# Kernel optimization log

Hardware: AMD Instinct MI355X
Metric: run time of the kernel (lower is better)

The kernel has to match this reference:

```python
import jax, jax.numpy as jnp
import numpy as np

CUTOFF = 5.0
N_RBF = 20
N_NODES, N_EDGES, F = 50000, 200000, 128


def setup_inputs() -> dict:
    key = jax.random.key(0)
    ks = jax.random.split(key, 11)
    inp = {
        "s": jax.random.normal(ks[0], (N_NODES, F), jnp.float32),
        "v": jax.random.normal(ks[1], (N_NODES, 3, F), jnp.float32),
        "rel_pos": jax.random.normal(ks[2], (N_EDGES, 3), jnp.float32),
        "W1": jax.random.normal(ks[3], (F, F), jnp.float32) * 0.05,
        "b1": jnp.zeros((F,), jnp.float32),
        "W2": jax.random.normal(ks[4], (F, 3 * F), jnp.float32) * 0.05,
        "b2": jnp.zeros((3 * F,), jnp.float32),
        "Wr": jax.random.normal(ks[5], (N_RBF, 3 * F), jnp.float32) * 0.05,
        "br": jnp.zeros((3 * F,), jnp.float32),
        "src": jax.random.randint(ks[6], (N_EDGES,), 0, N_NODES),
        "dst": jax.random.randint(ks[7], (N_EDGES,), 0, N_NODES),
    }
    return inp


def reference(s, v, rel_pos, W1, b1, W2, b2, Wr, br, src, dst):
    n_nodes, f = s.shape
    # phi MLP on node scalar features (computed per node, then gathered per edge)
    phi = jax.nn.silu(s @ W1 + b1) @ W2 + b2          # [N, 3F]
    phi_e = phi[src]                                   # [E, 3F]

    d = jnp.linalg.norm(rel_pos, axis=-1)              # [E]
    # sinc-style radial basis: sin(n*pi*d/cutoff)/d, n = 1..N_RBF
    n = jnp.arange(1, N_RBF + 1, dtype=d.dtype)
    rbf = jnp.sin(n * (jnp.pi / CUTOFF) * d[:, None]) / d[:, None]  # [E, 20]
    w_proj = rbf @ Wr + br                             # [E, 3F]
    # cosine cutoff gate
    fcut = 0.5 * (jnp.cos(jnp.pi * d / CUTOFF) + 1.0) * (d < CUTOFF)
    w = w_proj * fcut[:, None]                         # [E, 3F]

    split = w * phi_e                                  # hadamard gate, [E, 3F]
    s_v, s_s, s_r = split[:, :f], split[:, f:2 * f], split[:, 2 * f:]

    dirv = rel_pos / d[:, None]                        # r / ||r||, [E, 3]
    # vector message: gated neighbor vectors + gated directions
    dv = v[src] * s_v[:, None, :] + dirv[:, :, None] * s_r[:, None, :]  # [E,3,F]

    out_s = jax.ops.segment_sum(s_s, dst, num_segments=n_nodes)  # [N, F]
    out_v = jax.ops.segment_sum(dv, dst, num_segments=n_nodes)   # [N, 3, F]
    return out_v, out_s
```

## Files before the change

kernel.cpp:

```cpp
#include <hip/hip_runtime.h>
#include <math.h>

#define N_NODES_C 50000
#define N_EDGES_C 200000
#define FDIM 128
#define NRBF 20
#define CUT 5.0f
#define SC_BLK 196
#define GBLOCKS 6250
#define BATCH 32

typedef short  bf16x8 __attribute__((ext_vector_type(8)));
typedef float  f32x4  __attribute__((ext_vector_type(4)));
typedef unsigned int u32x3 __attribute__((ext_vector_type(3)));
typedef _Float16 f16x2 __attribute__((ext_vector_type(2)));

__device__ __forceinline__ unsigned short f32_to_bf16(float f) {
    unsigned u = __float_as_uint(f);
    unsigned r = (u + 0x7FFFu + ((u >> 16) & 1u)) >> 16;
    return (unsigned short)r;
}
__device__ __forceinline__ float bf16_to_f32(unsigned short h) {
    return __uint_as_float(((unsigned)h) << 16);
}
__device__ __forceinline__ unsigned short f16_bits(float x) {
    _Float16 h = (_Float16)x;
    unsigned short b;
    __builtin_memcpy(&b, &h, 2);
    return b;
}
__device__ __forceinline__ f16x2 u2h2(unsigned u) {
    f16x2 r;
    __builtin_memcpy(&r, &u, 4);
    return r;
}
__device__ __forceinline__ bf16x8 pack_bf16x8(f32x4 a, f32x4 b) {
    bf16x8 r;
    r[0] = (short)f32_to_bf16(a[0]); r[1] = (short)f32_to_bf16(a[1]);
    r[2] = (short)f32_to_bf16(a[2]); r[3] = (short)f32_to_bf16(a[3]);
    r[4] = (short)f32_to_bf16(b[0]); r[5] = (short)f32_to_bf16(b[1]);
    r[6] = (short)f32_to_bf16(b[2]); r[7] = (short)f32_to_bf16(b[3]);
    return r;
}

__global__ __launch_bounds__(256) void prep_all_kernel(
    const float* __restrict__ W1, const float* __restrict__ W2,
    const float* __restrict__ Wr, unsigned short* __restrict__ W1t,
    unsigned short* __restrict__ W2t, unsigned* __restrict__ wrh)
{
    int i = blockIdx.x * 256 + threadIdx.x;
    if (i < 128 * 128) {
        int n = i >> 7, k = i & 127;
        W1t[i] = f32_to_bf16(W1[k * 128 + n]);
    } else if (i < 128 * 128 + 384 * 128) {
        int j = i - 128 * 128;
        int n = j >> 7, k = j & 127;
        W2t[j] = f32_to_bf16(W2[k * 384 + n]);
    } else {
        int idx = i - (128 * 128 + 384 * 128);
        if (idx < 128 * 30) {
            int f  = idx / 30;
            int r  = idx % 30;
            int sec = r / 10, kp = r % 10;
            int col = sec * 128 + f;
            unsigned lo = f16_bits(Wr[(2 * kp)     * 384 + col]);
            unsigned hi = f16_bits(Wr[(2 * kp + 1) * 384 + col]);
            wrh[idx] = lo | (hi << 16);
        }
    }
}

__global__ __launch_bounds__(256) void vpack_kernel(
    const float* __restrict__ v, unsigned short* __restrict__ pv)
{
    const int total = N_NODES_C * 128;
    for (int idx = blockIdx.x * 256 + threadIdx.x; idx < total;
         idx += gridDim.x * 256) {
        int n = idx >> 7, f = idx & 127;
        const float* vr = v + (size_t)n * 384;
        unsigned short v0 = f32_to_bf16(__builtin_nontemporal_load(vr + f));
        unsigned short v1 = f32_to_bf16(__builtin_nontemporal_load(vr + 128 + f));
        unsigned short v2 = f32_to_bf16(__builtin_nontemporal_load(vr + 256 + f));
        char* base = (char*)pv + (size_t)n * 1536 + (size_t)f * 12;
        *(unsigned short*)(base + 6) = v0;
        *(unsigned*)(base + 8) = (unsigned)v1 | ((unsigned)v2 << 16);
    }
}

__global__ __launch_bounds__(256) void mlp1w_kernel(
    const float* __restrict__ s, const unsigned short* __restrict__ W1t,
    const float* __restrict__ b1, unsigned short* __restrict__ h)
{
    __shared__ unsigned short w1lds[128 * 136];

    const int tid = threadIdx.x;
#pragma unroll
    for (int j = 0; j < 8; ++j) {
        int fi = tid + j * 256;
        int row  = fi >> 4;
        int colq = fi & 15;
        *(float4*)&w1lds[row * 136 + colq * 8] =
            *(const float4*)(W1t + (size_t)fi * 8);
    }
    __syncthreads();

    const int wv = tid >> 6, lane = tid & 63;
    const int m0 = blockIdx.x * 64 + wv * 16;
    const int lr = lane & 15, lg = lane >> 4;
    int arow = m0 + lr; if (arow >= N_NODES_C) arow = N_NODES_C - 1;

    f32x4 acc[8];
#pragma unroll
    for (int nt = 0; nt < 8; ++nt) acc[nt] = (f32x4){0.f, 0.f, 0.f, 0.f};

#pragma unroll
    for (int kt = 0; kt < 4; ++kt) {
        const int k0 = kt * 32 + lg * 8;
        const f32x4* ap = (const f32x4*)(s + (size_t)arow * 128 + k0);
        f32x4 a0 = __builtin_nontemporal_load(ap);
        f32x4 a1 = __builtin_nontemporal_load(ap + 1);
        bf16x8 af = pack_bf16x8(a0, a1);
#pragma unroll
        for (int nt = 0; nt < 8; ++nt) {
            bf16x8 bf = *(const bf16x8*)&w1lds[(nt * 16 + lr) * 136 + k0];
            acc[nt] = __builtin_amdgcn_mfma_f32_16x16x32_bf16(af, bf, acc[nt], 0, 0, 0);
        }
    }

    const int crow = m0 + lg * 4;
#pragma unroll
    for (int nt = 0; nt < 8; ++nt) {
        int col = nt * 16 + lr;
        float bb = b1[col];
#pragma unroll
        for (int r = 0; r < 4; ++r) {
            int m = crow + r;
            if (m < N_NODES_C) {
                float x = acc[nt][r] + bb;
                x = x / (1.f + __expf(-x));
                h[(size_t)m * 128 + col] = f32_to_bf16(x);
            }
        }
    }
}

__global__ __launch_bounds__(256) void mlp2p_kernel(
    const unsigned short* __restrict__ h, const unsigned short* __restrict__ W2t,
    const float* __restrict__ b2, unsigned short* __restrict__ pv)
{
    __shared__ unsigned short wlds[2][3 * 16 * 136];

    const int tid = threadIdx.x;
    const int wv = tid >> 6, lane = tid & 63;
    const int rg = wv & 1;
    const int hf = wv >> 1;
    const int m0 = blockIdx.x * 32 + rg * 16;
    const int lr = lane & 15, lg = lane >> 4;
    int arow = m0 + lr; if (arow >= N_NODES_C) arow = N_NODES_C - 1;

    bf16x8 af2[4];
#pragma unroll
    for (int kt = 0; kt < 4; ++kt)
        af2[kt] = *(const bf16x8*)(h + (size_t)arow * 128 + kt * 32 + lg * 8);

    const int crow = m0 + lg * 4;

    for (int t = 0; t < 4; ++t) {
        __syncthreads();
#pragma unroll
        for (int j = 0; j < 6; ++j) {
            int fi = tid + j * 256;
            int half = (fi >= 768) ? 1 : 0;
            int rem  = fi - half * 768;
            int c    = rem >> 8;
            int r2   = rem & 255;
            int row  = r2 >> 4;
            int colq = r2 & 15;
            int nt   = half * 4 + t;
            *(float4*)&wlds[half][(c * 16 + row) * 136 + colq * 8] =
                *(const float4*)(W2t +
                    ((size_t)(c * 128 + nt * 16 + row) * 128 + colq * 8));
        }
        __syncthreads();

        const unsigned short* W = wlds[hf];
        f32x4 a0 = (f32x4){0.f, 0.f, 0.f, 0.f};
        f32x4 a1 = (f32x4){0.f, 0.f, 0.f, 0.f};
        f32x4 a2 = (f32x4){0.f, 0.f, 0.f, 0.f};
#pragma unroll
        for (int kt = 0; kt < 4; ++kt) {
            const int k0 = kt * 32 + lg * 8;
            bf16x8 bf0 = *(const bf16x8*)&W[(      lr) * 136 + k0];
            bf16x8 bf1 = *(const bf16x8*)&W[(16 +  lr) * 136 + k0];
            bf16x8 bf2 = *(const bf16x8*)&W[(32 +  lr) * 136 + k0];
            a0 = __builtin_amdgcn_mfma_f32_16x16x32_bf16(af2[kt], bf0, a0, 0, 0, 0);
            a1 = __builtin_amdgcn_mfma_f32_16x16x32_bf16(af2[kt], bf1, a1, 0, 0, 0);
            a2 = __builtin_amdgcn_mfma_f32_16x16x32_bf16(af2[kt], bf2, a2, 0, 0, 0);
        }

        const int col = (hf * 4 + t) * 16 + lr;
        const float bb0 = b2[col], bb1 = b2[128 + col], bb2 = b2[256 + col];
#pragma unroll
        for (int r = 0; r < 4; ++r) {
            int m = crow + r;
            if (m < N_NODES_C) {
                unsigned p0 = f32_to_bf16(a0[r] + bb0);
                unsigned p1 = f32_to_bf16(a1[r] + bb1);
                unsigned short p2 = f32_to_bf16(a2[r] + bb2);
                char* base = (char*)pv + (size_t)m * 1536 + (size_t)col * 12;
                *(unsigned*)(base) = p0 | (p1 << 16);
                *(unsigned short*)(base + 4) = p2;
            }
        }
    }
}

__global__ __launch_bounds__(256) void count_kernel(
    const int* __restrict__ dst, int* __restrict__ counts)
{
    int e = blockIdx.x * 256 + threadIdx.x;
    if (e < N_EDGES_C) atomicAdd(counts + dst[e], 1);
}

__global__ __launch_bounds__(256) void scan1_kernel(
    const int* __restrict__ counts, int* __restrict__ row_tmp,
    int* __restrict__ partial)
{
    __shared__ int sm[256];
    const int t = threadIdx.x;
    const int idx = blockIdx.x * 256 + t;
    int c = (idx < N_NODES_C) ? counts[idx] : 0;
    int x = c;
    sm[t] = x;
    __syncthreads();
#pragma unroll
    for (int off = 1; off < 256; off <<= 1) {
        int y = (t >= off) ? sm[t - off] : 0;
        __syncthreads();
        x += y;
        sm[t] = x;
        __syncthreads();
    }
    if (idx < N_NODES_C) row_tmp[idx] = x - c;
    if (t == 255) partial[blockIdx.x] = x;
}

__global__ __launch_bounds__(256) void scan2_kernel(
    const int* __restrict__ partial, int* __restrict__ poffs)
{
    __shared__ int sm[256];
    const int t = threadIdx.x;
    int c = (t < SC_BLK) ? partial[t] : 0;
    int x = c;
    sm[t] = x;
    __syncthreads();
#pragma unroll
    for (int off = 1; off < 256; off <<= 1) {
        int y = (t >= off) ? sm[t - off] : 0;
        __syncthreads();
        x += y;
        sm[t] = x;
        __syncthreads();
    }
    if (t < SC_BLK) poffs[t] = x - c;
}

__global__ __launch_bounds__(256) void scan3_kernel(
    const int* __restrict__ row_tmp, const int* __restrict__ poffs,
    int* __restrict__ row_ptr, int* __restrict__ row_fill)
{
    const int idx = blockIdx.x * 256 + threadIdx.x;
    if (idx < N_NODES_C) {
        int rp = row_tmp[idx] + poffs[blockIdx.x];
        row_ptr[idx]  = rp;
        row_fill[idx] = rp;
    }
    if (idx == 0) row_ptr[N_NODES_C] = N_EDGES_C;
}

__global__ __launch_bounds__(256) void fill_kernel(
    const float* __restrict__ rel_pos, const int* __restrict__ src,
    const int* __restrict__ dst, int* __restrict__ row_fill,
    float* __restrict__ e_meta)
{
    int e = blockIdx.x * 256 + threadIdx.x;
    if (e >= N_EDGES_C) return;

    int pos = atomicAdd(row_fill + dst[e], 1);

    float x = rel_pos[3 * e + 0];
    float y = rel_pos[3 * e + 1];
    float z = rel_pos[3 * e + 2];
    float d = sqrtf(x * x + y * y + z * z);
    float invd = 1.0f / d;

    float s1 = 0.f, c1 = 0.f, fcut = 0.f, amp = 0.f;
    if (d < CUT) {
        sincosf((3.14159265358979f / CUT) * d, &s1, &c1);
        fcut = 0.5f * (c1 + 1.0f);
        amp  = invd * fcut;
    }

    float rb[NRBF];
    float sk = s1, ck = c1;
#pragma unroll
    for (int k = 0; k < NRBF; ++k) {
        rb[k] = sk * amp;
        float sn = sk * c1 + ck * s1;
        ck = ck * c1 - sk * s1;
        sk = sn;
    }

    unsigned pk[10];
#pragma unroll
    for (int kp = 0; kp < 10; ++kp)
        pk[kp] = (unsigned)f16_bits(rb[2 * kp]) | ((unsigned)f16_bits(rb[2 * kp + 1]) << 16);

    float4* mp = (float4*)(e_meta + (size_t)pos * 16);
    mp[0] = make_float4(x * invd, y * invd, z * invd, fcut);
    mp[1] = make_float4(__uint_as_float(pk[0]), __uint_as_float(pk[1]),
                        __uint_as_float(pk[2]), __uint_as_float(pk[3]));
    mp[2] = make_float4(__uint_as_float(pk[4]), __uint_as_float(pk[5]),
                        __uint_as_float(pk[6]), __uint_as_float(pk[7]));
    mp[3] = make_float4(__uint_as_float(pk[8]), __uint_as_float(pk[9]),
                        __int_as_float(src[e]), 0.f);
}

#define COMPUTE_E(M_, U)                                                       \
    {                                                                          \
        const float4 m0 = *(const float4*)(M_);                                \
        const unsigned* mu_ = (const unsigned*)((M_) + 4);                     \
        float w0 = m0.w * br0, w1 = m0.w * br1, w2 = m0.w * br2;               \
        _Pragma("unroll")                                                      \
        for (int kp = 0; kp < 10; ++kp) {                                      \
            f16x2 rh = u2h2(mu_[kp]);                                          \
            w0 = __builtin_amdgcn_fdot2(rh, u2h2(wrp0[kp]), w0, false);        \
            w1 = __builtin_amdgcn_fdot2(rh, u2h2(wrp1[kp]), w1, false);        \
            w2 = __builtin_amdgcn_fdot2(rh, u2h2(wrp2[kp]), w2, false);        \
        }                                                                      \
        float P0 = bf16_to_f32((unsigned short)((U).x & 0xFFFFu));             \
        float P1 = bf16_to_f32((unsigned short)((U).x >> 16));                 \
        float P2 = bf16_to_f32((unsigned short)((U).y & 0xFFFFu));             \
        float V0 = bf16_to_f32((unsigned short)((U).y >> 16));                 \
        float V1 = bf16_to_f32((unsigned short)((U).z & 0xFFFFu));             \
        float V2 = bf16_to_f32((unsigned short)((U).z >> 16));                 \
        float sv = w0 * P0;                                                    \
        float ss = w1 * P1;                                                    \
        float sr = w2 * P2;                                                    \
        acc_s  += ss;                                                          \
        acc_v0 += V0 * sv + m0.x * sr;                                         \
        acc_v1 += V1 * sv + m0.y * sr;                                         \
        acc_v2 += V2 * sv + m0.z * sr;                                         \
    }

#define LOADPV(U, SI)                                                          \
    U = *(const u32x3*)((const char*)pv + (size_t)(SI) * 1536 + (size_t)f * 12);

#define STORE_NODE(N_, AS, A0, A1, A2)                                         \
    {                                                                          \
        __builtin_nontemporal_store(AS, &out_s[(size_t)(N_) * 128 + f]);       \
        __builtin_nontemporal_store(A0, &out_v[(size_t)(N_) * 384 +       f]); \
        __builtin_nontemporal_store(A1, &out_v[(size_t)(N_) * 384 + 128 + f]); \
        __builtin_nontemporal_store(A2, &out_v[(size_t)(N_) * 384 + 256 + f]); \
    }

#define BOUNDARY(GE)                                                           \
    if ((GE) + 1 == end_cur) {                                                 \
        STORE_NODE(cur, acc_s, acc_v0, acc_v1, acc_v2);                        \
        acc_s = acc_v0 = acc_v1 = acc_v2 = 0.f;                                \
        ++cur;                                                                 \
        while (cur < nhi) {                                                    \
            int ne_ = row_ptr[cur + 1];                                        \
            if (ne_ != (GE) + 1) { end_cur = ne_; break; }                     \
            STORE_NODE(cur, 0.f, 0.f, 0.f, 0.f);                               \
            ++cur;                                                             \
        }                                                                      \
    }

__global__ __launch_bounds__(128) void gather_packed_kernel(
    const unsigned short* __restrict__ pv, const unsigned* __restrict__ wrh,
    const float* __restrict__ br, const int* __restrict__ row_ptr,
    const float* __restrict__ e_meta,
    float* __restrict__ out_v, float* __restrict__ out_s)
{
    __shared__ float meta_lds[2][BATCH * 16];

    const int f = threadIdx.x;
    const int gid = blockIdx.x;
    const int chunk = (N_NODES_C + GBLOCKS - 1) / GBLOCKS;
    const int nlo = gid * chunk;
    if (nlo >= N_NODES_C) return;
    const int nhi = min(nlo + chunk, N_NODES_C);

    unsigned wrp0[10], wrp1[10], wrp2[10];
    {
        const unsigned* wp = wrh + (size_t)f * 30;
#pragma unroll
        for (int i = 0; i < 10; ++i) {
            wrp0[i] = wp[i];
            wrp1[i] = wp[10 + i];
            wrp2[i] = wp[20 + i];
        }
#pragma unroll
        for (int i = 0; i < 10; ++i)
            asm volatile("" : "+v"(wrp0[i]), "+v"(wrp1[i]), "+v"(wrp2[i]));
    }
    const float br0 = br[f], br1 = br[128 + f], br2 = br[256 + f];

    const int gbeg = row_ptr[nlo];
    const int gend = row_ptr[nhi];
    const int nedge = gend - gbeg;

    float acc_s = 0.f, acc_v0 = 0.f, acc_v1 = 0.f, acc_v2 = 0.f;

    int cur = nlo;
    while (cur < nhi && row_ptr[cur + 1] == gbeg) {
        STORE_NODE(cur, 0.f, 0.f, 0.f, 0.f);
        ++cur;
    }
    int end_cur = (cur < nhi) ? row_ptr[cur + 1] : gbeg;

    if (nedge > 0) {
        const f32x4* src0 = (const f32x4*)(e_meta + (size_t)gbeg * 16);
        f32x4 s0 = __builtin_nontemporal_load(src0 + threadIdx.x);
        ((f32x4*)meta_lds[0])[threadIdx.x] = s0;
    }
    __syncthreads();

    const int total_batches = (nedge + BATCH - 1) / BATCH;
    for (int b = 0; b < total_batches; ++b) {
        const int bstart = b * BATCH;
        const int bcount = min(BATCH, nedge - bstart);
        const bool have_next = (b + 1 < total_batches);

        f32x4 st;
        if (have_next) {
            const f32x4* srcn =
                (const f32x4*)(e_meta + (size_t)(gbeg + bstart + BATCH) * 16);
            st = __builtin_nontemporal_load(srcn + threadIdx.x);
        }

        const float* Mb = meta_lds[b & 1];

        u32x3 uA, uB;
        {
            int si = ((const int*)Mb)[14];
            LOADPV(uA, si);
        }

        int t = 0;
        while (t < bcount) {
            if (t + 1 < bcount) {
                int si = ((const int*)(Mb + (t + 1) * 16))[14];
                LOADPV(uB, si);
            }
            COMPUTE_E(Mb + t * 16, uA);
            BOUNDARY(gbeg + bstart + t);
            ++t; if (t >= bcount) break;

            if (t + 1 < bcount) {
                int si = ((const int*)(Mb + (t + 1) * 16))[14];
                LOADPV(uA, si);
            }
            COMPUTE_E(Mb + t * 16, uB);
            BOUNDARY(gbeg + bstart + t);
            ++t;
        }

        if (have_next) ((f32x4*)meta_lds[(b + 1) & 1])[threadIdx.x] = st;
        __syncthreads();
    }
}

extern "C" void kernel_launch(void* const* d_in, const int* in_sizes, int n_in,
                              void* d_out, int out_size, void* d_ws, size_t ws_size,
                              hipStream_t stream)
{
    const float* s  = (const float*)d_in[0];
    const float* v  = (const float*)d_in[1];
    const float* rp = (const float*)d_in[2];
    const float* W1 = (const float*)d_in[3];
    const float* b1 = (const float*)d_in[4];
    const float* W2 = (const float*)d_in[5];
    const float* b2 = (const float*)d_in[6];
    const float* Wr = (const float*)d_in[7];
    const float* br = (const float*)d_in[8];
    const int* src  = (const int*)d_in[9];
    const int* dst  = (const int*)d_in[10];

    float* out   = (float*)d_out;
    float* out_v = out;
    float* out_s = out + (size_t)N_NODES_C * 3 * FDIM;

    char* ws = (char*)d_ws;
    float* e_meta = (float*)ws;                 ws += ((size_t)N_EDGES_C * 16 + 256) * sizeof(float);
    unsigned short* W1t = (unsigned short*)ws;  ws += (size_t)128 * 128 * sizeof(unsigned short);
    unsigned short* W2t = (unsigned short*)ws;  ws += (size_t)384 * 128 * sizeof(unsigned short);
    unsigned* wrh = (unsigned*)ws;              ws += (size_t)128 * 30 * sizeof(unsigned);
    int* counts   = (int*)ws;                   ws += (size_t)N_NODES_C * sizeof(int);
    int* row_ptr  = (int*)ws;                   ws += (size_t)(N_NODES_C + 4) * sizeof(int);
    int* row_fill = (int*)ws;                   ws += (size_t)N_NODES_C * sizeof(int);
    int* row_tmp  = (int*)ws;                   ws += (size_t)N_NODES_C * sizeof(int);
    int* partial  = (int*)ws;                   ws += (size_t)256 * sizeof(int);
    int* poffs    = (int*)ws;                   ws += (size_t)256 * sizeof(int);
    unsigned short* h = (unsigned short*)ws;    ws += (size_t)N_NODES_C * 128 * sizeof(unsigned short);
    unsigned short* pv = (unsigned short*)ws;

    hipMemsetAsync(counts, 0, (size_t)N_NODES_C * sizeof(int), stream);

    count_kernel<<<(N_EDGES_C + 255) / 256, 256, 0, stream>>>(dst, counts);
    scan1_kernel<<<SC_BLK, 256, 0, stream>>>(counts, row_tmp, partial);
    scan2_kernel<<<1, 256, 0, stream>>>(partial, poffs);
    scan3_kernel<<<SC_BLK, 256, 0, stream>>>(row_tmp, poffs, row_ptr, row_fill);
    fill_kernel<<<(N_EDGES_C + 255) / 256, 256, 0, stream>>>(rp, src, dst, row_fill, e_meta);

    prep_all_kernel<<<272, 256, 0, stream>>>(W1, W2, Wr, W1t, W2t, wrh);
    vpack_kernel<<<4096, 256, 0, stream>>>(v, pv);
    mlp1w_kernel<<<(N_NODES_C + 63) / 64, 256, 0, stream>>>(s, W1t, b1, h);
    mlp2p_kernel<<<(N_NODES_C + 31) / 32, 256, 0, stream>>>(h, W2t, b2, pv);

    gather_packed_kernel<<<GBLOCKS, 128, 0, stream>>>(pv, wrh, br, row_ptr,
                                                      e_meta, out_v, out_s);
}
```

Before: 200.7 us.

## Merge independent preprocessing kernels into two block-partitioned launches

Folds vpack, count, and weight prep into one launch whose blocks are split by role. It also folds mlp1 and the edge fill into a second launch, cutting the launch count from 10 to 7. The goal is to remove launch gaps and let independent work run at the same time on the GPU. The cost is that k5 blocks all reserve the shared memory sized for the MLP branch, which may lower occupancy for the fill blocks.

```diff
diff --git a/kernel.cpp b/kernel.cpp
--- a/kernel.cpp
+++ b/kernel.cpp
@@ -10,6 +10,12 @@
 #define GBLOCKS 6250
 #define BATCH 32
 
+#define K1_VP 4096
+#define K1_CT 782
+#define K1_PR 272
+#define K5_ML 782
+#define K5_FL 782
+
 typedef short  bf16x8 __attribute__((ext_vector_type(8)));
 typedef float  f32x4  __attribute__((ext_vector_type(4)));
 typedef unsigned int u32x3 __attribute__((ext_vector_type(3)));
@@ -43,104 +49,214 @@
     return r;
 }
 
-__global__ __launch_bounds__(256) void prep_all_kernel(
+__global__ __launch_bounds__(256) void k1_kernel(
+    const float* __restrict__ v, unsigned short* __restrict__ pv,
+    const int* __restrict__ dst, int* __restrict__ counts,
     const float* __restrict__ W1, const float* __restrict__ W2,
     const float* __restrict__ Wr, unsigned short* __restrict__ W1t,
     unsigned short* __restrict__ W2t, unsigned* __restrict__ wrh)
 {
-    int i = blockIdx.x * 256 + threadIdx.x;
-    if (i < 128 * 128) {
-        int n = i >> 7, k = i & 127;
-        W1t[i] = f32_to_bf16(W1[k * 128 + n]);
-    } else if (i < 128 * 128 + 384 * 128) {
-        int j = i - 128 * 128;
-        int n = j >> 7, k = j & 127;
-        W2t[j] = f32_to_bf16(W2[k * 384 + n]);
+    const int bid = blockIdx.x;
+    const int tid = threadIdx.x;
+
+    if (bid < K1_VP) {
+        const int total = N_NODES_C * 128;
+        for (int idx = bid * 256 + tid; idx < total; idx += K1_VP * 256) {
+            int n = idx >> 7, f = idx & 127;
+            const float* vr = v + (size_t)n * 384;
+            unsigned short v0 = f32_to_bf16(__builtin_nontemporal_load(vr + f));
+            unsigned short v1 = f32_to_bf16(__builtin_nontemporal_load(vr + 128 + f));
+            unsigned short v2 = f32_to_bf16(__builtin_nontemporal_load(vr + 256 + f));
+            char* base = (char*)pv + (size_t)n * 1536 + (size_t)f * 12;
+            *(unsigned short*)(base + 6) = v0;
+            *(unsigned*)(base + 8) = (unsigned)v1 | ((unsigned)v2 << 16);
+        }
+    } else if (bid < K1_VP + K1_CT) {
+        int e = (bid - K1_VP) * 256 + tid;
+        if (e < N_EDGES_C) atomicAdd(counts + dst[e], 1);
     } else {
-        int idx = i - (128 * 128 + 384 * 128);
-        if (idx < 128 * 30) {
-            int f  = idx / 30;
-            int r  = idx % 30;
-            int sec = r / 10, kp = r % 10;
-            int col = sec * 128 + f;
-            unsigned lo = f16_bits(Wr[(2 * kp)     * 384 + col]);
-            unsigned hi = f16_bits(Wr[(2 * kp + 1) * 384 + col]);
-            wrh[idx] = lo | (hi << 16);
-        }
-    }
-}
-
-__global__ __launch_bounds__(256) void vpack_kernel(
-    const float* __restrict__ v, unsigned short* __restrict__ pv)
-{
-    const int total = N_NODES_C * 128;
-    for (int idx = blockIdx.x * 256 + threadIdx.x; idx < total;
-         idx += gridDim.x * 256) {
-        int n = idx >> 7, f = idx & 127;
-        const float* vr = v + (size_t)n * 384;
-        unsigned short v0 = f32_to_bf16(__builtin_nontemporal_load(vr + f));
-        unsigned short v1 = f32_to_bf16(__builtin_nontemporal_load(vr + 128 + f));
-        unsigned short v2 = f32_to_bf16(__builtin_nontemporal_load(vr + 256 + f));
-        char* base = (char*)pv + (size_t)n * 1536 + (size_t)f * 12;
-        *(unsigned short*)(base + 6) = v0;
-        *(unsigned*)(base + 8) = (unsigned)v1 | ((unsigned)v2 << 16);
-    }
-}
-
-__global__ __launch_bounds__(256) void mlp1w_kernel(
+        int i = (bid - K1_VP - K1_CT) * 256 + tid;
+        if (i < 128 * 128) {
+            int n = i >> 7, k = i & 127;
+            W1t[i] = f32_to_bf16(W1[k * 128 + n]);
+        } else if (i < 128 * 128 + 384 * 128) {
+            int j = i - 128 * 128;
+            int n = j >> 7, k = j & 127;
+            W2t[j] = f32_to_bf16(W2[k * 384 + n]);
+        } else {
+            int idx = i - (128 * 128 + 384 * 128);
+            if (idx < 128 * 30) {
+                int f  = idx / 30;
+                int r  = idx % 30;
+                int sec = r / 10, kp = r % 10;
+                int col = sec * 128 + f;
+                unsigned lo = f16_bits(Wr[(2 * kp)     * 384 + col]);
+                unsigned hi = f16_bits(Wr[(2 * kp + 1) * 384 + col]);
+                wrh[idx] = lo | (hi << 16);
+            }
+        }
+    }
+}
+
+__global__ __launch_bounds__(256) void scan1_kernel(
+    const int* __restrict__ counts, int* __restrict__ row_tmp,
+    int* __restrict__ partial)
+{
+    __shared__ int sm[256];
+    const int t = threadIdx.x;
+    const int idx = blockIdx.x * 256 + t;
+    int c = (idx < N_NODES_C) ? counts[idx] : 0;
+    int x = c;
+    sm[t] = x;
+    __syncthreads();
+#pragma unroll
+    for (int off = 1; off < 256; off <<= 1) {
+        int y = (t >= off) ? sm[t - off] : 0;
+        __syncthreads();
+        x += y;
+        sm[t] = x;
+        __syncthreads();
+    }
+    if (idx < N_NODES_C) row_tmp[idx] = x - c;
+    if (t == 255) partial[blockIdx.x] = x;
+}
+
+__global__ __launch_bounds__(256) void scan2_kernel(
+    const int* __restrict__ partial, int* __restrict__ poffs)
+{
+    __shared__ int sm[256];
+    const int t = threadIdx.x;
+    int c = (t < SC_BLK) ? partial[t] : 0;
+    int x = c;
+    sm[t] = x;
+    __syncthreads();
+#pragma unroll
+    for (int off = 1; off < 256; off <<= 1) {
+        int y = (t >= off) ? sm[t - off] : 0;
+        __syncthreads();
+        x += y;
+        sm[t] = x;
+        __syncthreads();
+    }
+    if (t < SC_BLK) poffs[t] = x - c;
+}
+
+__global__ __launch_bounds__(256) void scan3_kernel(
+    const int* __restrict__ row_tmp, const int* __restrict__ poffs,
+    int* __restrict__ row_ptr, int* __restrict__ row_fill)
+{
+    const int idx = blockIdx.x * 256 + threadIdx.x;
+    if (idx < N_NODES_C) {
+        int rp = row_tmp[idx] + poffs[blockIdx.x];
+        row_ptr[idx]  = rp;
+        row_fill[idx] = rp;
+    }
+    if (idx == 0) row_ptr[N_NODES_C] = N_EDGES_C;
+}
+
+__global__ __launch_bounds__(256) void k5_kernel(
     const float* __restrict__ s, const unsigned short* __restrict__ W1t,
-    const float* __restrict__ b1, unsigned short* __restrict__ h)
+    const float* __restrict__ b1, unsigned short* __restrict__ h,
+    const float* __restrict__ rel_pos, const int* __restrict__ src,
+    const int* __restrict__ dst, int* __restrict__ row_fill,
+    float* __restrict__ e_meta)
 {
     __shared__ unsigned short w1lds[128 * 136];
 
+    const int bid = blockIdx.x;
     const int tid = threadIdx.x;
-#pragma unroll
-    for (int j = 0; j < 8; ++j) {
-        int fi = tid + j * 256;
-        int row  = fi >> 4;
-        int colq = fi & 15;
-        *(float4*)&w1lds[row * 136 + colq * 8] =
-            *(const float4*)(W1t + (size_t)fi * 8);
-    }
-    __syncthreads();
-
-    const int wv = tid >> 6, lane = tid & 63;
-    const int m0 = blockIdx.x * 64 + wv * 16;
-    const int lr = lane & 15, lg = lane >> 4;
-    int arow = m0 + lr; if (arow >= N_NODES_C) arow = N_NODES_C - 1;
-
-    f32x4 acc[8];
-#pragma unroll
-    for (int nt = 0; nt < 8; ++nt) acc[nt] = (f32x4){0.f, 0.f, 0.f, 0.f};
-
-#pragma unroll
-    for (int kt = 0; kt < 4; ++kt) {
-        const int k0 = kt * 32 + lg * 8;
-        const f32x4* ap = (const f32x4*)(s + (size_t)arow * 128 + k0);
-        f32x4 a0 = __builtin_nontemporal_load(ap);
-        f32x4 a1 = __builtin_nontemporal_load(ap + 1);
-        bf16x8 af = pack_bf16x8(a0, a1);
+
+    if (bid < K5_ML) {
+#pragma unroll
+        for (int j = 0; j < 8; ++j) {
+            int fi = tid + j * 256;
+            int row  = fi >> 4;
+            int colq = fi & 15;
+            *(float4*)&w1lds[row * 136 + colq * 8] =
+                *(const float4*)(W1t + (size_t)fi * 8);
+        }
+        __syncthreads();
+
+        const int wv = tid >> 6, lane = tid & 63;
+        const int m0 = bid * 64 + wv * 16;
+        const int lr = lane & 15, lg = lane >> 4;
+        int arow = m0 + lr; if (arow >= N_NODES_C) arow = N_NODES_C - 1;
+
+        f32x4 acc[8];
+#pragma unroll
+        for (int nt = 0; nt < 8; ++nt) acc[nt] = (f32x4){0.f, 0.f, 0.f, 0.f};
+
+#pragma unroll
+        for (int kt = 0; kt < 4; ++kt) {
+            const int k0 = kt * 32 + lg * 8;
+            const f32x4* ap = (const f32x4*)(s + (size_t)arow * 128 + k0);
+            f32x4 a0 = __builtin_nontemporal_load(ap);
+            f32x4 a1 = __builtin_nontemporal_load(ap + 1);
+            bf16x8 af = pack_bf16x8(a0, a1);
+#pragma unroll
+            for (int nt = 0; nt < 8; ++nt) {
+                bf16x8 bf = *(const bf16x8*)&w1lds[(nt * 16 + lr) * 136 + k0];
+                acc[nt] = __builtin_amdgcn_mfma_f32_16x16x32_bf16(af, bf, acc[nt], 0, 0, 0);
+            }
+        }
+
+        const int crow = m0 + lg * 4;
 #pragma unroll
         for (int nt = 0; nt < 8; ++nt) {
-            bf16x8 bf = *(const bf16x8*)&w1lds[(nt * 16 + lr) * 136 + k0];
-            acc[nt] = __builtin_amdgcn_mfma_f32_16x16x32_bf16(af, bf, acc[nt], 0, 0, 0);
-        }
-    }
-
-    const int crow = m0 + lg * 4;
-#pragma unroll
-    for (int nt = 0; nt < 8; ++nt) {
-        int col = nt * 16 + lr;
-        float bb = b1[col];
-#pragma unroll
-        for (int r = 0; r < 4; ++r) {
-            int m = crow + r;
-            if (m < N_NODES_C) {
-                float x = acc[nt][r] + bb;
-                x = x / (1.f + __expf(-x));
-                h[(size_t)m * 128 + col] = f32_to_bf16(x);
+            int col = nt * 16 + lr;
+            float bb = b1[col];
+#pragma unroll
+            for (int r = 0; r < 4; ++r) {
+                int m = crow + r;
+                if (m < N_NODES_C) {
+                    float x = acc[nt][r] + bb;
+                    x = x / (1.f + __expf(-x));
+                    h[(size_t)m * 128 + col] = f32_to_bf16(x);
+                }
             }
         }
+    } else {
+        int e = (bid - K5_ML) * 256 + tid;
+        if (e >= N_EDGES_C) return;
+
+        int pos = atomicAdd(row_fill + dst[e], 1);
+
+        float x = rel_pos[3 * e + 0];
+        float y = rel_pos[3 * e + 1];
+        float z = rel_pos[3 * e + 2];
+        float d = sqrtf(x * x + y * y + z * z);
+        float invd = 1.0f / d;
+
+        float s1 = 0.f, c1 = 0.f, fcut = 0.f, amp = 0.f;
+        if (d < CUT) {
+            sincosf((3.14159265358979f / CUT) * d, &s1, &c1);
+            fcut = 0.5f * (c1 + 1.0f);
+            amp  = invd * fcut;
+        }
+
+        float rb[NRBF];
+        float sk = s1, ck = c1;
+#pragma unroll
+        for (int k = 0; k < NRBF; ++k) {
+            rb[k] = sk * amp;
+            float sn = sk * c1 + ck * s1;
+            ck = ck * c1 - sk * s1;
+            sk = sn;
+        }
+
+        unsigned pk[10];
+#pragma unroll
+        for (int kp = 0; kp < 10; ++kp)
+            pk[kp] = (unsigned)f16_bits(rb[2 * kp]) | ((unsigned)f16_bits(rb[2 * kp + 1]) << 16);
+
+        float4* mp = (float4*)(e_meta + (size_t)pos * 16);
+        mp[0] = make_float4(x * invd, y * invd, z * invd, fcut);
+        mp[1] = make_float4(__uint_as_float(pk[0]), __uint_as_float(pk[1]),
+                            __uint_as_float(pk[2]), __uint_as_float(pk[3]));
+        mp[2] = make_float4(__uint_as_float(pk[4]), __uint_as_float(pk[5]),
+                            __uint_as_float(pk[6]), __uint_as_float(pk[7]));
+        mp[3] = make_float4(__uint_as_float(pk[8]), __uint_as_float(pk[9]),
+                            __int_as_float(src[e]), 0.f);
     }
 }
 
@@ -213,117 +329,6 @@
             }
         }
     }
-}
-
-__global__ __launch_bounds__(256) void count_kernel(
-    const int* __restrict__ dst, int* __restrict__ counts)
-{
-    int e = blockIdx.x * 256 + threadIdx.x;
-    if (e < N_EDGES_C) atomicAdd(counts + dst[e], 1);
-}
-
-__global__ __launch_bounds__(256) void scan1_kernel(
-    const int* __restrict__ counts, int* __restrict__ row_tmp,
-    int* __restrict__ partial)
-{
-    __shared__ int sm[256];
-    const int t = threadIdx.x;
-    const int idx = blockIdx.x * 256 + t;
-    int c = (idx < N_NODES_C) ? counts[idx] : 0;
-    int x = c;
-    sm[t] = x;
-    __syncthreads();
-#pragma unroll
-    for (int off = 1; off < 256; off <<= 1) {
-        int y = (t >= off) ? sm[t - off] : 0;
-        __syncthreads();
-        x += y;
-        sm[t] = x;
-        __syncthreads();
-    }
-    if (idx < N_NODES_C) row_tmp[idx] = x - c;
-    if (t == 255) partial[blockIdx.x] = x;
-}
-
-__global__ __launch_bounds__(256) void scan2_kernel(
-    const int* __restrict__ partial, int* __restrict__ poffs)
-{
-    __shared__ int sm[256];
-    const int t = threadIdx.x;
-    int c = (t < SC_BLK) ? partial[t] : 0;
-    int x = c;
-    sm[t] = x;
-    __syncthreads();
-#pragma unroll
-    for (int off = 1; off < 256; off <<= 1) {
-        int y = (t >= off) ? sm[t - off] : 0;
-        __syncthreads();
-        x += y;
-        sm[t] = x;
-        __syncthreads();
-    }
-    if (t < SC_BLK) poffs[t] = x - c;
-}
-
-__global__ __launch_bounds__(256) void scan3_kernel(
-    const int* __restrict__ row_tmp, const int* __restrict__ poffs,
-    int* __restrict__ row_ptr, int* __restrict__ row_fill)
-{
-    const int idx = blockIdx.x * 256 + threadIdx.x;
-    if (idx < N_NODES_C) {
-        int rp = row_tmp[idx] + poffs[blockIdx.x];
-        row_ptr[idx]  = rp;
-        row_fill[idx] = rp;
-    }
-    if (idx == 0) row_ptr[N_NODES_C] = N_EDGES_C;
-}
-
-__global__ __launch_bounds__(256) void fill_kernel(
-    const float* __restrict__ rel_pos, const int* __restrict__ src,
-    const int* __restrict__ dst, int* __restrict__ row_fill,
-    float* __restrict__ e_meta)
-{
-    int e = blockIdx.x * 256 + threadIdx.x;
-    if (e >= N_EDGES_C) return;
-
-    int pos = atomicAdd(row_fill + dst[e], 1);
-
-    float x = rel_pos[3 * e + 0];
-    float y = rel_pos[3 * e + 1];
-    float z = rel_pos[3 * e + 2];
-    float d = sqrtf(x * x + y * y + z * z);
-    float invd = 1.0f / d;
-
-    float s1 = 0.f, c1 = 0.f, fcut = 0.f, amp = 0.f;
-    if (d < CUT) {
-        sincosf((3.14159265358979f / CUT) * d, &s1, &c1);
-        fcut = 0.5f * (c1 + 1.0f);
-        amp  = invd * fcut;
-    }
-
-    float rb[NRBF];
-    float sk = s1, ck = c1;
-#pragma unroll
-    for (int k = 0; k < NRBF; ++k) {
-        rb[k] = sk * amp;
-        float sn = sk * c1 + ck * s1;
-        ck = ck * c1 - sk * s1;
-        sk = sn;
-    }
-
-    unsigned pk[10];
-#pragma unroll
-    for (int kp = 0; kp < 10; ++kp)
-        pk[kp] = (unsigned)f16_bits(rb[2 * kp]) | ((unsigned)f16_bits(rb[2 * kp + 1]) << 16);
-
-    float4* mp = (float4*)(e_meta + (size_t)pos * 16);
-    mp[0] = make_float4(x * invd, y * invd, z * invd, fcut);
-    mp[1] = make_float4(__uint_as_float(pk[0]), __uint_as_float(pk[1]),
-                        __uint_as_float(pk[2]), __uint_as_float(pk[3]));
-    mp[2] = make_float4(__uint_as_float(pk[4]), __uint_as_float(pk[5]),
-                        __uint_as_float(pk[6]), __uint_as_float(pk[7]));
-    mp[3] = make_float4(__uint_as_float(pk[8]), __uint_as_float(pk[9]),
-                        __int_as_float(src[e]), 0.f);
 }
 
 #define COMPUTE_E(M_, U)                                                       \
@@ -508,15 +513,13 @@
 
     hipMemsetAsync(counts, 0, (size_t)N_NODES_C * sizeof(int), stream);
 
-    count_kernel<<<(N_EDGES_C + 255) / 256, 256, 0, stream>>>(dst, counts);
+    k1_kernel<<<K1_VP + K1_CT + K1_PR, 256, 0, stream>>>(
+        v, pv, dst, counts, W1, W2, Wr, W1t, W2t, wrh);
     scan1_kernel<<<SC_BLK, 256, 0, stream>>>(counts, row_tmp, partial);
     scan2_kernel<<<1, 256, 0, stream>>>(partial, poffs);
     scan3_kernel<<<SC_BLK, 256, 0, stream>>>(row_tmp, poffs, row_ptr, row_fill);
-    fill_kernel<<<(N_EDGES_C + 255) / 256, 256, 0, stream>>>(rp, src, dst, row_fill, e_meta);
-
-    prep_all_kernel<<<272, 256, 0, stream>>>(W1, W2, Wr, W1t, W2t, wrh);
-    vpack_kernel<<<4096, 256, 0, stream>>>(v, pv);
-    mlp1w_kernel<<<(N_NODES_C + 63) / 64, 256, 0, stream>>>(s, W1t, b1, h);
+    k5_kernel<<<K5_ML + K5_FL, 256, 0, stream>>>(
+        s, W1t, b1, h, rp, src, dst, row_fill, e_meta);
     mlp2p_kernel<<<(N_NODES_C + 31) / 32, 256, 0, stream>>>(h, W2t, b2, pv);
 
     gather_packed_kernel<<<GBLOCKS, 128, 0, stream>>>(pv, wrh, br, row_ptr,
```

Result: faster. 185.6 us (-7.6%).
